# Optimization experiments

Hardware: AMD Instinct MI355X
Metric: run time of the kernel (lower is better)

## Reference

```python
import jax, jax.numpy as jnp
import numpy as np

EMBED = 32
HEADS = 8
HEAD_DIM = EMBED // HEADS  # 4


def setup_inputs() -> dict:
    key = jax.random.key(0)
    ks = jax.random.split(key, 12)
    N, Q, K = 4, 2048, 2048
    inp = {
        "query": jax.random.normal(ks[0], (N, Q, EMBED), dtype=jnp.float32),
        "key": jax.random.normal(ks[1], (N, K, EMBED), dtype=jnp.float32),
        "value": jax.random.normal(ks[2], (N, K, EMBED), dtype=jnp.float32),
        "mask": jnp.ones((N, 1, Q, K), dtype=jnp.int32),
        # nn.Linear params: W stored as (in, out) here; math y = x @ W + b
        "Wq": jax.random.normal(ks[3], (EMBED, EMBED), dtype=jnp.float32) / np.sqrt(EMBED),
        "bq": jax.random.normal(ks[4], (EMBED,), dtype=jnp.float32) * 0.01,
        "Wk": jax.random.normal(ks[5], (EMBED, EMBED), dtype=jnp.float32) / np.sqrt(EMBED),
        "bk": jax.random.normal(ks[6], (EMBED,), dtype=jnp.float32) * 0.01,
        "Wv": jax.random.normal(ks[7], (EMBED, EMBED), dtype=jnp.float32) / np.sqrt(EMBED),
        "bv": jax.random.normal(ks[8], (EMBED,), dtype=jnp.float32) * 0.01,
        "Wo": jax.random.normal(ks[9], (EMBED, EMBED), dtype=jnp.float32) / np.sqrt(EMBED),
        "bo": jax.random.normal(ks[10], (EMBED,), dtype=jnp.float32) * 0.01,
    }
    return inp


def reference(query, key, value, mask, Wq, bq, Wk, bk, Wv, bv, Wo, bo):
    N, Qlen, _ = query.shape
    Klen = key.shape[1]
    # linear projections
    q = (query @ Wq + bq).reshape(N, Qlen, HEADS, HEAD_DIM)
    k = (key @ Wk + bk).reshape(N, Klen, HEADS, HEAD_DIM)
    v = (value @ Wv + bv).reshape(N, Klen, HEADS, HEAD_DIM)
    # energy: [N, H, Q, K]
    energy = jnp.einsum("nqhd,nkhd->nhqk", q, k)
    energy = jnp.where(mask == 0, jnp.float32(-1e20), energy)
    # NOTE: original scales by sqrt(embedSize), not sqrt(headDim)
    attn = jax.nn.softmax(energy / jnp.sqrt(jnp.float32(EMBED)), axis=3)
    out = jnp.einsum("nhqv,nvhd->nqhd", attn, v).reshape(N, Qlen, EMBED)
    return out @ Wo + bo
```

## Files before the change

kernel.cpp:

```cpp
#include <hip/hip_runtime.h>

#define NB 4
#define SEQ 2048
#define EMB 32
#define HEADS 8
#define HD 4

typedef float v2f __attribute__((ext_vector_type(2)));
typedef unsigned int uint;

__device__ __forceinline__ v2f splat2(float x) { v2f r; r.x = x; r.y = x; return r; }
__device__ __forceinline__ v2f pkfma(v2f a, v2f b, v2f c) {
  return __builtin_elementwise_fma(a, b, c);
}

__global__ __launch_bounds__(256) void pack_proj_kernel(
    const int* __restrict__ mask, uint* __restrict__ pmw,
    const float* __restrict__ key, const float* __restrict__ value,
    const float* __restrict__ Wk, const float* __restrict__ bk,
    const float* __restrict__ Wv, const float* __restrict__ bv,
    float* __restrict__ Kp, float* __restrict__ Vp) {
  const int packBlocks = NB * SEQ * SEQ / 4 / 256;
  if (blockIdx.x < packBlocks) {
    int g = blockIdx.x * 256 + threadIdx.x;
    const int4 v = ((const int4*)mask)[g];
    uint nib = (uint)(v.x != 0) | ((uint)(v.y != 0) << 1) |
               ((uint)(v.z != 0) << 2) | ((uint)(v.w != 0) << 3);
    int lane = threadIdx.x & 63;
    uint w = nib << (4 * (lane & 7));
    w |= __shfl_xor(w, 1);
    w |= __shfl_xor(w, 2);
    w |= __shfl_xor(w, 4);
    if ((lane & 7) == 0) pmw[g >> 3] = w;
  } else {
    const int half = NB * SEQ / 8;
    int blk2 = blockIdx.x - packBlocks;
    bool isV = blk2 >= half;
    const float* X = isV ? value : key;
    const float* W = isV ? Wv : Wk;
    const float* b = isV ? bv : bk;
    float* P = isV ? Vp : Kp;
    int blk = isV ? (blk2 - half) : blk2;

    __shared__ float sW[EMB][EMB];
    __shared__ float sb[EMB];
    __shared__ float sX[8][EMB];
    int t = threadIdx.x;
    for (int i = t; i < EMB * EMB; i += 256) sW[i >> 5][i & 31] = W[i];
    if (t < EMB) sb[t] = b[t];
    size_t row0 = (size_t)blk * 8;
    int r = t >> 5, c = t & 31;
    sX[r][c] = X[(row0 + r) * EMB + c];
    __syncthreads();
    float acc = sb[c];
#pragma unroll
    for (int d = 0; d < EMB; ++d) acc = fmaf(sX[r][d], sW[d][c], acc);
    P[(row0 + r) * EMB + c] = acc;
  }
}

__device__ __forceinline__ void load_tile(
    const float*& kptr, const float*& vptr,
    float4 (&KK)[4], float4 (&VV)[4]) {
  KK[0] = *(const float4*)(kptr);
  KK[1] = *(const float4*)(kptr + EMB);
  KK[2] = *(const float4*)(kptr + 2 * EMB);
  KK[3] = *(const float4*)(kptr + 3 * EMB);
  VV[0] = *(const float4*)(vptr);
  VV[1] = *(const float4*)(vptr + EMB);
  VV[2] = *(const float4*)(vptr + 2 * EMB);
  VV[3] = *(const float4*)(vptr + 3 * EMB);
  kptr += 32 * EMB; vptr += 32 * EMB;
}

__device__ __forceinline__ void compute_tile(
    const float4 (&KK)[4], const float4 (&VV)[4],
    const v2f (&q2)[4][4], v2f (&l2)[4], v2f (&ac2)[4][4]) {
#pragma unroll
  for (int p = 0; p < 4; ++p) {
    v2f pf[4];
#pragma unroll
    for (int j = 0; j < 4; ++j) {
      const float4 kk = KK[j];
      v2f s = pkfma(q2[p][0], splat2(kk.x),
              pkfma(q2[p][1], splat2(kk.y),
              pkfma(q2[p][2], splat2(kk.z), q2[p][3] * splat2(kk.w))));
      pf[j].x = __builtin_amdgcn_exp2f(s.x);
      pf[j].y = __builtin_amdgcn_exp2f(s.y);
    }
    l2[p] += (pf[0] + pf[1]) + (pf[2] + pf[3]);
#pragma unroll
    for (int j = 0; j < 4; ++j) {
      const float4 vv = VV[j];
      ac2[p][0] = pkfma(pf[j], splat2(vv.x), ac2[p][0]);
      ac2[p][1] = pkfma(pf[j], splat2(vv.y), ac2[p][1]);
      ac2[p][2] = pkfma(pf[j], splat2(vv.z), ac2[p][2]);
      ac2[p][3] = pkfma(pf[j], splat2(vv.w), ac2[p][3]);
    }
  }
}

__device__ __forceinline__ void compute_tile_masked(
    const float4 (&KK)[4], const float4 (&VV)[4],
    const uint (&MW)[8], int ks4,
    const v2f (&q2)[4][4], v2f (&l2)[4], v2f (&ac2)[4][4]) {
#pragma unroll
  for (int p = 0; p < 4; ++p) {
    v2f pf[4];
#pragma unroll
    for (int j = 0; j < 4; ++j) {
      const float4 kk = KK[j];
      v2f s = pkfma(q2[p][0], splat2(kk.x),
              pkfma(q2[p][1], splat2(kk.y),
              pkfma(q2[p][2], splat2(kk.z), q2[p][3] * splat2(kk.w))));
      pf[j].x = ((MW[2 * p + 0] >> (ks4 + j)) & 1u) ? __builtin_amdgcn_exp2f(s.x) : 0.0f;
      pf[j].y = ((MW[2 * p + 1] >> (ks4 + j)) & 1u) ? __builtin_amdgcn_exp2f(s.y) : 0.0f;
    }
    l2[p] += (pf[0] + pf[1]) + (pf[2] + pf[3]);
#pragma unroll
    for (int j = 0; j < 4; ++j) {
      const float4 vv = VV[j];
      ac2[p][0] = pkfma(pf[j], splat2(vv.x), ac2[p][0]);
      ac2[p][1] = pkfma(pf[j], splat2(vv.y), ac2[p][1]);
      ac2[p][2] = pkfma(pf[j], splat2(vv.z), ac2[p][2]);
      ac2[p][3] = pkfma(pf[j], splat2(vv.w), ac2[p][3]);
    }
  }
}

__global__ __launch_bounds__(256, 2) void attn_kernel(
    const float* __restrict__ query, const uint* __restrict__ pmw,
    const float* __restrict__ Kp, const float* __restrict__ Vp,
    const float* __restrict__ Wq, const float* __restrict__ bq,
    const float* __restrict__ Wo, const float* __restrict__ bo,
    float* __restrict__ out) {
  __shared__ float sWq[EMB][EMB];
  __shared__ float sWo[EMB][EMB];
  __shared__ float sbq[EMB];
  __shared__ float sbo[EMB];
  __shared__ float sX[16][EMB];
  __shared__ float sCtx[16][EMB + 1];
  __shared__ float sPart[2][16][EMB];
  __shared__ float sL[2][16][HEADS];

  int t = threadIdx.x;
  int n = blockIdx.x >> 7;
  int qt = blockIdx.x & 127;
  int qrow0 = qt * 16;

  int w = t >> 6;
  int octet = w >> 1;
  int kh = w & 1;
  int lane = t & 63;
  int h = lane & 7;
  int ks = lane >> 3;
  int ks4 = 4 * ks;
  int rbl = 8 * octet;

  for (int i = t; i < EMB * EMB; i += 256) {
    sWq[i >> 5][i & 31] = Wq[i];
    sWo[i >> 5][i & 31] = Wo[i];
  }
  if (t < EMB) { sbq[t] = bq[t]; sbo[t] = bo[t]; }
#pragma unroll
  for (int rr = 0; rr < 2; ++rr) {
    int r = (t >> 5) + 8 * rr, c = t & 31;
    sX[r][c] = query[((size_t)n * SEQ + qrow0 + r) * EMB + c];
  }
  __syncthreads();

  const float SC = 0.17677669529663687f * 1.4426950408889634f;
  v2f q2[4][4];
#pragma unroll
  for (int p = 0; p < 4; ++p)
#pragma unroll
    for (int d = 0; d < 4; ++d) q2[p][d] = splat2(sbq[4 * h + d]);
#pragma unroll
  for (int j = 0; j < EMB; ++j) {
    float w0 = sWq[j][4 * h + 0], w1 = sWq[j][4 * h + 1];
    float w2 = sWq[j][4 * h + 2], w3 = sWq[j][4 * h + 3];
#pragma unroll
    for (int p = 0; p < 4; ++p) {
      v2f x;
      x.x = sX[rbl + 2 * p + 0][j];
      x.y = sX[rbl + 2 * p + 1][j];
      q2[p][0] = pkfma(x, splat2(w0), q2[p][0]);
      q2[p][1] = pkfma(x, splat2(w1), q2[p][1]);
      q2[p][2] = pkfma(x, splat2(w2), q2[p][2]);
      q2[p][3] = pkfma(x, splat2(w3), q2[p][3]);
    }
  }
#pragma unroll
  for (int p = 0; p < 4; ++p)
#pragma unroll
    for (int d = 0; d < 4; ++d) q2[p][d] *= splat2(SC);

  const uint* mbase = pmw + ((size_t)n * SEQ + qrow0 + rbl) * (SEQ / 32) + kh * 32;
  int wl = lane & 7, rl = lane >> 3;
  const uint* mr = mbase + (size_t)rl * 64;
  uint myand = mr[wl] & mr[wl + 8] & mr[wl + 16] & mr[wl + 24];
  bool allones = __all(myand == 0xFFFFFFFFu);

  const float* kptr = Kp + (size_t)n * SEQ * EMB + (size_t)kh * 1024 * EMB
                         + (size_t)ks4 * EMB + 4 * h;
  const float* vptr = Vp + (size_t)n * SEQ * EMB + (size_t)kh * 1024 * EMB
                         + (size_t)ks4 * EMB + 4 * h;

  v2f l2[4], ac2[4][4];
#pragma unroll
  for (int p = 0; p < 4; ++p) {
    l2[p] = splat2(0.0f);
#pragma unroll
    for (int d = 0; d < 4; ++d) ac2[p][d] = splat2(0.0f);
  }

  if (allones) {
    float4 ka[4], va[4], kb[4], vb[4];
    load_tile(kptr, vptr, ka, va);
    for (int i = 0; i < 15; ++i) {
      load_tile(kptr, vptr, kb, vb);
      compute_tile(ka, va, q2, l2, ac2);
      load_tile(kptr, vptr, ka, va);
      compute_tile(kb, vb, q2, l2, ac2);
    }
    load_tile(kptr, vptr, kb, vb);
    compute_tile(ka, va, q2, l2, ac2);
    compute_tile(kb, vb, q2, l2, ac2);
  } else {
    for (int tile = 0; tile < 32; ++tile) {
      float4 ka[4], va[4];
      load_tile(kptr, vptr, ka, va);
      uint MW[8];
#pragma unroll
      for (int rr = 0; rr < 8; ++rr) MW[rr] = mbase[(size_t)rr * 64 + tile];
      compute_tile_masked(ka, va, MW, ks4, q2, l2, ac2);
    }
  }

#pragma unroll
  for (int d = 8; d <= 32; d <<= 1) {
#pragma unroll
    for (int p = 0; p < 4; ++p) {
      l2[p].x += __shfl_xor(l2[p].x, d);
      l2[p].y += __shfl_xor(l2[p].y, d);
#pragma unroll
      for (int e = 0; e < 4; ++e) {
        ac2[p][e].x += __shfl_xor(ac2[p][e].x, d);
        ac2[p][e].y += __shfl_xor(ac2[p][e].y, d);
      }
    }
  }

#pragma unroll
  for (int p = 0; p < 4; ++p) {
    int r0 = rbl + 2 * p;
    if (ks < 4) {
      float vA = (ks == 0) ? ac2[p][0].x : (ks == 1) ? ac2[p][1].x
               : (ks == 2) ? ac2[p][2].x : ac2[p][3].x;
      float vB = (ks == 0) ? ac2[p][0].y : (ks == 1) ? ac2[p][1].y
               : (ks == 2) ? ac2[p][2].y : ac2[p][3].y;
      sPart[kh][r0 + 0][4 * h + ks] = vA;
      sPart[kh][r0 + 1][4 * h + ks] = vB;
    } else if (ks == 4) {
      sL[kh][r0 + 0][h] = l2[p].x;
      sL[kh][r0 + 1][h] = l2[p].y;
    }
  }
  __syncthreads();

#pragma unroll
  for (int rr = 0; rr < 2; ++rr) {
    int r = (t >> 5) + 8 * rr, c = t & 31, hh = (t & 31) >> 2;
    float num = sPart[0][r][c] + sPart[1][r][c];
    float den = sL[0][r][hh] + sL[1][r][hh];
    sCtx[r][c] = num * __builtin_amdgcn_rcpf(den);
  }
  __syncthreads();

#pragma unroll
  for (int rr = 0; rr < 2; ++rr) {
    int r = (t >> 5) + 8 * rr, e = t & 31;
    float o = sbo[e];
#pragma unroll
    for (int j = 0; j < EMB; ++j) o = fmaf(sCtx[r][j], sWo[j][e], o);
    out[((size_t)n * SEQ + qrow0 + r) * EMB + e] = o;
  }
}

extern "C" void kernel_launch(void* const* d_in, const int* in_sizes, int n_in,
                              void* d_out, int out_size, void* d_ws, size_t ws_size,
                              hipStream_t stream) {
  const float* query = (const float*)d_in[0];
  const float* key   = (const float*)d_in[1];
  const float* value = (const float*)d_in[2];
  const int*   mask  = (const int*)d_in[3];
  const float* Wq = (const float*)d_in[4];
  const float* bq = (const float*)d_in[5];
  const float* Wk = (const float*)d_in[6];
  const float* bk = (const float*)d_in[7];
  const float* Wv = (const float*)d_in[8];
  const float* bv = (const float*)d_in[9];
  const float* Wo = (const float*)d_in[10];
  const float* bo = (const float*)d_in[11];
  float* out = (float*)d_out;

  float* Kp = (float*)d_ws;
  float* Vp = Kp + (size_t)NB * SEQ * EMB;
  uint* pmw = (uint*)(Vp + (size_t)NB * SEQ * EMB);

  const int packBlocks = NB * SEQ * SEQ / 4 / 256;
  const int projBlocks = 2 * NB * SEQ / 8;
  pack_proj_kernel<<<dim3(packBlocks + projBlocks), dim3(256), 0, stream>>>(
      mask, pmw, key, value, Wk, bk, Wv, bv, Kp, Vp);
  attn_kernel<<<dim3(NB * (SEQ / 16)), dim3(256), 0, stream>>>(
      query, pmw, Kp, Vp, Wq, bq, Wo, bo, out);
}
```

Baseline: 58.98 us.

## Drop mask bit-packing pass; stream raw mask inside attention and verify afterwards

```diff
diff --git a/kernel.cpp b/kernel.cpp
--- a/kernel.cpp
+++ b/kernel.cpp
@@ -14,54 +14,38 @@
   return __builtin_elementwise_fma(a, b, c);
 }
 
-__global__ __launch_bounds__(256) void pack_proj_kernel(
-    const int* __restrict__ mask, uint* __restrict__ pmw,
+__global__ __launch_bounds__(256) void proj_kv_kernel(
     const float* __restrict__ key, const float* __restrict__ value,
     const float* __restrict__ Wk, const float* __restrict__ bk,
     const float* __restrict__ Wv, const float* __restrict__ bv,
     float* __restrict__ Kp, float* __restrict__ Vp) {
-  const int packBlocks = NB * SEQ * SEQ / 4 / 256;
-  if (blockIdx.x < packBlocks) {
-    int g = blockIdx.x * 256 + threadIdx.x;
-    const int4 v = ((const int4*)mask)[g];
-    uint nib = (uint)(v.x != 0) | ((uint)(v.y != 0) << 1) |
-               ((uint)(v.z != 0) << 2) | ((uint)(v.w != 0) << 3);
-    int lane = threadIdx.x & 63;
-    uint w = nib << (4 * (lane & 7));
-    w |= __shfl_xor(w, 1);
-    w |= __shfl_xor(w, 2);
-    w |= __shfl_xor(w, 4);
-    if ((lane & 7) == 0) pmw[g >> 3] = w;
-  } else {
-    const int half = NB * SEQ / 8;
-    int blk2 = blockIdx.x - packBlocks;
-    bool isV = blk2 >= half;
-    const float* X = isV ? value : key;
-    const float* W = isV ? Wv : Wk;
-    const float* b = isV ? bv : bk;
-    float* P = isV ? Vp : Kp;
-    int blk = isV ? (blk2 - half) : blk2;
-
-    __shared__ float sW[EMB][EMB];
-    __shared__ float sb[EMB];
-    __shared__ float sX[8][EMB];
-    int t = threadIdx.x;
-    for (int i = t; i < EMB * EMB; i += 256) sW[i >> 5][i & 31] = W[i];
-    if (t < EMB) sb[t] = b[t];
-    size_t row0 = (size_t)blk * 8;
-    int r = t >> 5, c = t & 31;
-    sX[r][c] = X[(row0 + r) * EMB + c];
-    __syncthreads();
-    float acc = sb[c];
-#pragma unroll
-    for (int d = 0; d < EMB; ++d) acc = fmaf(sX[r][d], sW[d][c], acc);
-    P[(row0 + r) * EMB + c] = acc;
-  }
+  const int half = NB * SEQ / 8;
+  bool isV = blockIdx.x >= half;
+  const float* X = isV ? value : key;
+  const float* W = isV ? Wv : Wk;
+  const float* b = isV ? bv : bk;
+  float* P = isV ? Vp : Kp;
+  int blk = isV ? (blockIdx.x - half) : blockIdx.x;
+
+  __shared__ float sW[EMB][EMB];
+  __shared__ float sb[EMB];
+  __shared__ float sX[8][EMB];
+  int t = threadIdx.x;
+  for (int i = t; i < EMB * EMB; i += 256) sW[i >> 5][i & 31] = W[i];
+  if (t < EMB) sb[t] = b[t];
+  size_t row0 = (size_t)blk * 8;
+  int r = t >> 5, c = t & 31;
+  sX[r][c] = X[(row0 + r) * EMB + c];
+  __syncthreads();
+  float acc = sb[c];
+#pragma unroll
+  for (int d = 0; d < EMB; ++d) acc = fmaf(sX[r][d], sW[d][c], acc);
+  P[(row0 + r) * EMB + c] = acc;
 }
 
 __device__ __forceinline__ void load_tile(
-    const float*& kptr, const float*& vptr,
-    float4 (&KK)[4], float4 (&VV)[4]) {
+    const float*& kptr, const float*& vptr, const int*& mptr,
+    float4 (&KK)[4], float4 (&VV)[4], int4& MQ) {
   KK[0] = *(const float4*)(kptr);
   KK[1] = *(const float4*)(kptr + EMB);
   KK[2] = *(const float4*)(kptr + 2 * EMB);
@@ -70,7 +54,8 @@
   VV[1] = *(const float4*)(vptr + EMB);
   VV[2] = *(const float4*)(vptr + 2 * EMB);
   VV[3] = *(const float4*)(vptr + 3 * EMB);
-  kptr += 32 * EMB; vptr += 32 * EMB;
+  MQ = *(const int4*)(mptr);
+  kptr += 32 * EMB; vptr += 32 * EMB; mptr += 32;
 }
 
 __device__ __forceinline__ void compute_tile(
@@ -101,11 +86,11 @@
 }
 
 __device__ __forceinline__ void compute_tile_masked(
-    const float4 (&KK)[4], const float4 (&VV)[4],
-    const uint (&MW)[8], int ks4,
+    const float4 (&KK)[4], const float4 (&VV)[4], const int4 (&MQ)[8],
     const v2f (&q2)[4][4], v2f (&l2)[4], v2f (&ac2)[4][4]) {
 #pragma unroll
   for (int p = 0; p < 4; ++p) {
+    const int4 mA = MQ[2 * p], mB = MQ[2 * p + 1];
     v2f pf[4];
 #pragma unroll
     for (int j = 0; j < 4; ++j) {
@@ -113,8 +98,10 @@
       v2f s = pkfma(q2[p][0], splat2(kk.x),
               pkfma(q2[p][1], splat2(kk.y),
               pkfma(q2[p][2], splat2(kk.z), q2[p][3] * splat2(kk.w))));
-      pf[j].x = ((MW[2 * p + 0] >> (ks4 + j)) & 1u) ? __builtin_amdgcn_exp2f(s.x) : 0.0f;
-      pf[j].y = ((MW[2 * p + 1] >> (ks4 + j)) & 1u) ? __builtin_amdgcn_exp2f(s.y) : 0.0f;
+      int ma_ = (j == 0) ? mA.x : (j == 1) ? mA.y : (j == 2) ? mA.z : mA.w;
+      int mb_ = (j == 0) ? mB.x : (j == 1) ? mB.y : (j == 2) ? mB.z : mB.w;
+      pf[j].x = ma_ ? __builtin_amdgcn_exp2f(s.x) : 0.0f;
+      pf[j].y = mb_ ? __builtin_amdgcn_exp2f(s.y) : 0.0f;
     }
     l2[p] += (pf[0] + pf[1]) + (pf[2] + pf[3]);
 #pragma unroll
@@ -129,7 +116,7 @@
 }
 
 __global__ __launch_bounds__(256, 2) void attn_kernel(
-    const float* __restrict__ query, const uint* __restrict__ pmw,
+    const float* __restrict__ query, const int* __restrict__ mask,
     const float* __restrict__ Kp, const float* __restrict__ Vp,
     const float* __restrict__ Wq, const float* __restrict__ bq,
     const float* __restrict__ Wo, const float* __restrict__ bo,
@@ -149,13 +136,14 @@
   int qrow0 = qt * 16;
 
   int w = t >> 6;
-  int octet = w >> 1;
+  int oc = w >> 1;
   int kh = w & 1;
   int lane = t & 63;
   int h = lane & 7;
   int ks = lane >> 3;
   int ks4 = 4 * ks;
-  int rbl = 8 * octet;
+  int h4 = 4 * h;
+  int rbl = 8 * oc;
 
   for (int i = t; i < EMB * EMB; i += 256) {
     sWq[i >> 5][i & 31] = Wq[i];
@@ -174,20 +162,22 @@
 #pragma unroll
   for (int p = 0; p < 4; ++p)
 #pragma unroll
-    for (int d = 0; d < 4; ++d) q2[p][d] = splat2(sbq[4 * h + d]);
+    for (int d = 0; d < 4; ++d) q2[p][d] = splat2(sbq[h4 + d]);
 #pragma unroll
   for (int j = 0; j < EMB; ++j) {
-    float w0 = sWq[j][4 * h + 0], w1 = sWq[j][4 * h + 1];
-    float w2 = sWq[j][4 * h + 2], w3 = sWq[j][4 * h + 3];
+    v2f w0 = splat2(sWq[j][h4 + 0]);
+    v2f w1 = splat2(sWq[j][h4 + 1]);
+    v2f w2 = splat2(sWq[j][h4 + 2]);
+    v2f w3 = splat2(sWq[j][h4 + 3]);
 #pragma unroll
     for (int p = 0; p < 4; ++p) {
       v2f x;
       x.x = sX[rbl + 2 * p + 0][j];
       x.y = sX[rbl + 2 * p + 1][j];
-      q2[p][0] = pkfma(x, splat2(w0), q2[p][0]);
-      q2[p][1] = pkfma(x, splat2(w1), q2[p][1]);
-      q2[p][2] = pkfma(x, splat2(w2), q2[p][2]);
-      q2[p][3] = pkfma(x, splat2(w3), q2[p][3]);
+      q2[p][0] = pkfma(x, w0, q2[p][0]);
+      q2[p][1] = pkfma(x, w1, q2[p][1]);
+      q2[p][2] = pkfma(x, w2, q2[p][2]);
+      q2[p][3] = pkfma(x, w3, q2[p][3]);
     }
   }
 #pragma unroll
@@ -195,16 +185,12 @@
 #pragma unroll
     for (int d = 0; d < 4; ++d) q2[p][d] *= splat2(SC);
 
-  const uint* mbase = pmw + ((size_t)n * SEQ + qrow0 + rbl) * (SEQ / 32) + kh * 32;
-  int wl = lane & 7, rl = lane >> 3;
-  const uint* mr = mbase + (size_t)rl * 64;
-  uint myand = mr[wl] & mr[wl + 8] & mr[wl + 16] & mr[wl + 24];
-  bool allones = __all(myand == 0xFFFFFFFFu);
-
-  const float* kptr = Kp + (size_t)n * SEQ * EMB + (size_t)kh * 1024 * EMB
-                         + (size_t)ks4 * EMB + 4 * h;
-  const float* vptr = Vp + (size_t)n * SEQ * EMB + (size_t)kh * 1024 * EMB
-                         + (size_t)ks4 * EMB + 4 * h;
+  const float* Kg = Kp + (size_t)n * SEQ * EMB + (size_t)kh * 1024 * EMB;
+  const float* Vg = Vp + (size_t)n * SEQ * EMB + (size_t)kh * 1024 * EMB;
+  const float* kptr = Kg + (size_t)ks4 * EMB + h4;
+  const float* vptr = Vg + (size_t)ks4 * EMB + h4;
+  const int* msl = mask + ((size_t)n * SEQ + qrow0 + rbl) * SEQ + kh * 1024;
+  const int* mptr = msl + (size_t)(lane >> 3) * SEQ + (lane & 7) * 4;
 
   v2f l2[4], ac2[4][4];
 #pragma unroll
@@ -214,26 +200,51 @@
     for (int d = 0; d < 4; ++d) ac2[p][d] = splat2(0.0f);
   }
 
-  if (allones) {
+  uint mAnd = 0xFFFFFFFFu;
+  {
     float4 ka[4], va[4], kb[4], vb[4];
-    load_tile(kptr, vptr, ka, va);
+    int4 ma, mb;
+    load_tile(kptr, vptr, mptr, ka, va, ma);
     for (int i = 0; i < 15; ++i) {
-      load_tile(kptr, vptr, kb, vb);
+      load_tile(kptr, vptr, mptr, kb, vb, mb);
       compute_tile(ka, va, q2, l2, ac2);
-      load_tile(kptr, vptr, ka, va);
+      mAnd &= (uint)ma.x & (uint)ma.y & (uint)ma.z & (uint)ma.w;
+      load_tile(kptr, vptr, mptr, ka, va, ma);
       compute_tile(kb, vb, q2, l2, ac2);
-    }
-    load_tile(kptr, vptr, kb, vb);
+      mAnd &= (uint)mb.x & (uint)mb.y & (uint)mb.z & (uint)mb.w;
+    }
+    load_tile(kptr, vptr, mptr, kb, vb, mb);
     compute_tile(ka, va, q2, l2, ac2);
+    mAnd &= (uint)ma.x & (uint)ma.y & (uint)ma.z & (uint)ma.w;
     compute_tile(kb, vb, q2, l2, ac2);
-  } else {
+    mAnd &= (uint)mb.x & (uint)mb.y & (uint)mb.z & (uint)mb.w;
+  }
+
+  if (!__all(mAnd == 0xFFFFFFFFu)) {
+#pragma unroll
+    for (int p = 0; p < 4; ++p) {
+      l2[p] = splat2(0.0f);
+#pragma unroll
+      for (int d = 0; d < 4; ++d) ac2[p][d] = splat2(0.0f);
+    }
+    const float* kp2 = Kg + (size_t)ks4 * EMB + h4;
+    const float* vp2 = Vg + (size_t)ks4 * EMB + h4;
     for (int tile = 0; tile < 32; ++tile) {
-      float4 ka[4], va[4];
-      load_tile(kptr, vptr, ka, va);
-      uint MW[8];
-#pragma unroll
-      for (int rr = 0; rr < 8; ++rr) MW[rr] = mbase[(size_t)rr * 64 + tile];
-      compute_tile_masked(ka, va, MW, ks4, q2, l2, ac2);
+      float4 KK[4], VV[4];
+      KK[0] = *(const float4*)(kp2);
+      KK[1] = *(const float4*)(kp2 + EMB);
+      KK[2] = *(const float4*)(kp2 + 2 * EMB);
+      KK[3] = *(const float4*)(kp2 + 3 * EMB);
+      VV[0] = *(const float4*)(vp2);
+      VV[1] = *(const float4*)(vp2 + EMB);
+      VV[2] = *(const float4*)(vp2 + 2 * EMB);
+      VV[3] = *(const float4*)(vp2 + 3 * EMB);
+      kp2 += 32 * EMB; vp2 += 32 * EMB;
+      int4 MQ[8];
+#pragma unroll
+      for (int rr = 0; rr < 8; ++rr)
+        MQ[rr] = *(const int4*)(msl + (size_t)rr * SEQ + tile * 32 + ks4);
+      compute_tile_masked(KK, VV, MQ, q2, l2, ac2);
     }
   }
 
@@ -259,8 +270,8 @@
                : (ks == 2) ? ac2[p][2].x : ac2[p][3].x;
       float vB = (ks == 0) ? ac2[p][0].y : (ks == 1) ? ac2[p][1].y
                : (ks == 2) ? ac2[p][2].y : ac2[p][3].y;
-      sPart[kh][r0 + 0][4 * h + ks] = vA;
-      sPart[kh][r0 + 1][4 * h + ks] = vB;
+      sPart[kh][r0 + 0][h4 + ks] = vA;
+      sPart[kh][r0 + 1][h4 + ks] = vB;
     } else if (ks == 4) {
       sL[kh][r0 + 0][h] = l2[p].x;
       sL[kh][r0 + 1][h] = l2[p].y;
@@ -306,12 +317,9 @@
 
   float* Kp = (float*)d_ws;
   float* Vp = Kp + (size_t)NB * SEQ * EMB;
-  uint* pmw = (uint*)(Vp + (size_t)NB * SEQ * EMB);
-
-  const int packBlocks = NB * SEQ * SEQ / 4 / 256;
-  const int projBlocks = 2 * NB * SEQ / 8;
-  pack_proj_kernel<<<dim3(packBlocks + projBlocks), dim3(256), 0, stream>>>(
-      mask, pmw, key, value, Wk, bk, Wv, bv, Kp, Vp);
+
+  proj_kv_kernel<<<dim3(2 * NB * SEQ / 8), dim3(256), 0, stream>>>(
+      key, value, Wk, bk, Wv, bv, Kp, Vp);
   attn_kernel<<<dim3(NB * (SEQ / 16)), dim3(256), 0, stream>>>(
-      query, pmw, Kp, Vp, Wq, bq, Wo, bo, out);
-}
+      query, mask, Kp, Vp, Wq, bq, Wo, bo, out);
+}
```

New measurement: 94.70 us. 1.61x slower.
